# Performance work log

Measured on AMD Instinct MI355X. Metric: run time of the kernel, lower is better.

Reference implementation:

```python
import jax, jax.numpy as jnp
import numpy as np
from jax.scipy.special import logsumexp

B, K = 256, 6144            # batch, info block length (n = 3K, rate 1/3)
NUM_ITER = 6
MU = 3                      # memory of RSC code (constraint_length 4)
NS = 1 << MU                # 8 trellis states
G0 = (1, 0, 1, 1)           # feedback polynomial '1011'
G1 = (1, 1, 0, 1)           # output polynomial  '1101'
NEG = -1e30


def _build_trellis():
    nxt = np.zeros((NS, 2), np.int32)
    par = np.zeros((NS, 2), np.int32)
    for s in range(NS):
        r = [(s >> (MU - 1 - j)) & 1 for j in range(MU)]  # r[0] newest register bit
        for u in (0, 1):
            fb = (u + sum(G0[j + 1] * r[j] for j in range(MU))) % 2
            p = (G1[0] * fb + sum(G1[j + 1] * r[j] for j in range(MU))) % 2
            nxt[s, u] = (fb << (MU - 1)) | (s >> 1)
            par[s, u] = p
    prev_s = np.zeros((NS, 2), np.int32)
    prev_u = np.zeros((NS, 2), np.int32)
    cnt = np.zeros(NS, np.int32)
    for s in range(NS):
        for u in (0, 1):
            sn = nxt[s, u]
            prev_s[sn, cnt[sn]] = s
            prev_u[sn, cnt[sn]] = u
            cnt[sn] += 1
    return nxt, par, prev_s, prev_u

_NXT, _PAR, _PREV_S, _PREV_U = _build_trellis()


def bcjr(l_sys, l_par, l_a):
    """log-MAP BCJR on the rate-1/2 RSC trellis. LLR convention log p(0)/p(1).
    l_sys, l_par, l_a: [B, K] -> posterior LLR [B, K]."""
    nxt = jnp.asarray(_NXT)
    prev_s = jnp.asarray(_PREV_S)
    prev_u = jnp.asarray(_PREV_U)
    par_sign = jnp.asarray(1.0 - 2.0 * _PAR, l_sys.dtype)  # [NS,2]
    u_sign = jnp.asarray([1.0, -1.0], l_sys.dtype)         # (1-2u)
    b = l_sys.shape[0]
    lsu = (l_sys + l_a).T                                  # [K,B]
    lp = l_par.T
    # branch metrics gamma[t, b, s, u] = 0.5*((1-2u)(Lsys+La) + (1-2p)Lpar)
    gamma = 0.5 * (lsu[:, :, None, None] * u_sign + lp[:, :, None, None] * par_sign)
    alpha0 = jnp.full((b, NS), NEG, l_sys.dtype).at[:, 0].set(0.0)  # start in state 0

    def fwd(alpha, g):
        a = logsumexp(alpha[:, prev_s] + g[:, prev_s, prev_u], axis=-1)  # [B,NS]
        a = a - jnp.max(a, axis=-1, keepdims=True)
        return a, alpha

    _, alphas = jax.lax.scan(fwd, alpha0, gamma)           # alphas[t] = alpha_t  [K,B,NS]
    beta_end = jnp.zeros((b, NS), l_sys.dtype)             # unterminated: uniform

    def bwd(beta, g):
        bn = logsumexp(g + beta[:, nxt], axis=-1)          # [B,NS]
        bn = bn - jnp.max(bn, axis=-1, keepdims=True)
        return bn, beta

    _, betas1 = jax.lax.scan(bwd, beta_end, gamma, reverse=True)  # betas1[t] = beta_{t+1}
    m = alphas[..., None] + gamma + betas1[:, :, nxt]      # [K,B,NS,2]
    l_post = logsumexp(m[..., 0], axis=-1) - logsumexp(m[..., 1], axis=-1)  # [K,B]
    return l_post.T


def turbo_decode(inputs, perm):
    llr = -inputs                 # sionna logits log p1/p0 -> internal LLR log p0/p1
    ls1 = llr[:, 0::3]            # systematic
    lp1 = llr[:, 1::3]            # parity of encoder 1
    lp2 = llr[:, 2::3]            # parity of encoder 2
    ls2 = ls1[:, perm]            # interleaved systematic for decoder 2
    inv = jnp.argsort(perm)       # deinterleave index
    le2_de = jnp.zeros_like(ls1)
    for _ in range(NUM_ITER):
        la1 = le2_de
        lpost1 = bcjr(ls1, lp1, la1)
        le1 = lpost1 - la1 - ls1                  # extrinsic of decoder 1
        la2 = le1[:, perm]
        lpost2 = bcjr(ls2, lp2, la2)
        le2_de = (lpost2 - la2 - ls2)[:, inv]     # deinterleaved extrinsic of decoder 2
    return -lpost2[:, inv]        # soft output, back to logit convention (hard_out=False)


def setup_inputs() -> dict:
    key = jax.random.key(0)
    k1, k2 = jax.random.split(key)
    inputs = jax.random.normal(k1, (B, 3 * K), dtype=jnp.float32)
    perm = jax.random.permutation(k2, K)
    return {"inputs": inputs, "perm": perm}


def reference(inputs, perm):
    return turbo_decode(inputs, perm)
```

## Files before the change

### kernel.cpp

```cpp
#include <hip/hip_runtime.h>
#include <hip/hip_fp16.h>

constexpr int B_ = 256;
constexpr int K_ = 6144;
constexpr int NITER = 6;
constexpr int L_ = 6;
constexpr int W0_ = 6;
constexpr int C_ = K_ / L_;
constexpr int CPB = 4;
constexpr int GRID = C_ / CPB;
constexpr float LOG2E = 1.4426950408889634f;
constexpr float LN2   = 0.6931471805599453f;

static_assert(K_ % L_ == 0, "");
static_assert((L_ % 2) == 0 && (W0_ % 2) == 0, "");
static_assert(W0_ <= L_, "uniform-warmup trick requires W0 <= L");
static_assert(C_ % CPB == 0, "");

#if __has_builtin(__builtin_amdgcn_exp2f)
#define EXP2F(x) __builtin_amdgcn_exp2f(x)
#else
#define EXP2F(x) exp2f(x)
#endif
#if __has_builtin(__builtin_amdgcn_logf)
#define LOG2F(x) __builtin_amdgcn_logf(x)
#else
#define LOG2F(x) log2f(x)
#endif
#if __has_builtin(__builtin_amdgcn_rcpf)
#define RCPF(x) __builtin_amdgcn_rcpf(x)
#else
#define RCPF(x) (1.0f / (x))
#endif

__device__ __forceinline__ float b2f(unsigned short u) {
  return __uint_as_float((unsigned)u << 16);
}
__device__ __forceinline__ unsigned short f2b(float f) {
  unsigned u = __float_as_uint(f);
  u += 0x7FFFu + ((u >> 16) & 1u);
  return (unsigned short)(u >> 16);
}
__device__ __forceinline__ float h2f_bits(unsigned short us) {
  __half_raw r; r.x = us; return __half2float(__half(r));
}
__device__ __forceinline__ unsigned short f2h_bits(float f) {
  return __half_as_ushort(__float2half(f));
}

__device__ __forceinline__ unsigned int ld_dev_u32(const unsigned int* p) {
  return __hip_atomic_load(const_cast<unsigned int*>(p), __ATOMIC_RELAXED,
                           __HIP_MEMORY_SCOPE_AGENT);
}
__device__ __forceinline__ void st_dev_u32(unsigned int* p, unsigned int v) {
  __hip_atomic_store(p, v, __ATOMIC_RELAXED, __HIP_MEMORY_SCOPE_AGENT);
}
__device__ __forceinline__ float ld_dev_f32(const float* p) {
  return __hip_atomic_load(const_cast<float*>(p), __ATOMIC_RELAXED,
                           __HIP_MEMORY_SCOPE_AGENT);
}
__device__ __forceinline__ void st_dev_f32(float* p, float v) {
  __hip_atomic_store(p, v, __ATOMIC_RELAXED, __HIP_MEMORY_SCOPE_AGENT);
}
__device__ __forceinline__ unsigned long long ld_dev_u64(
    const unsigned long long* p) {
  return __hip_atomic_load(const_cast<unsigned long long*>(p),
                           __ATOMIC_RELAXED, __HIP_MEMORY_SCOPE_AGENT);
}
__device__ __forceinline__ void st_dev_u64(unsigned long long* p,
                                           unsigned long long v) {
  __hip_atomic_store(p, v, __ATOMIC_RELAXED, __HIP_MEMORY_SCOPE_AGENT);
}

__device__ __forceinline__ void gam_lin(float gxv, float gyv, float g[4]) {
  float es = EXP2F(-fabsf(gxv));
  float ep = EXP2F(-fabsf(gyv));
  float fu0 = gxv >= 0.0f ? 1.0f : es;
  float fu1 = gxv >= 0.0f ? es : 1.0f;
  float fp0 = gyv >= 0.0f ? 1.0f : ep;
  float fp1 = gyv >= 0.0f ? ep : 1.0f;
  g[0] = fu0 * fp0; g[1] = fu0 * fp1;
  g[2] = fu1 * fp0; g[3] = fu1 * fp1;
}

__device__ __forceinline__ void step_fwd_lin(float a[8], const float g[4]) {
  float an[8];
#pragma unroll
  for (int sn = 0; sn < 8; ++sn) {
    const int u0 = ((sn >> 2) ^ (sn & 1)) & 1;
    const int p0 = ((sn >> 2) ^ ((sn >> 1) & 1)) & 1;
    an[sn] = a[(sn & 3) * 2] * g[u0 * 2 + p0]
           + a[(sn & 3) * 2 + 1] * g[(u0 ^ 1) * 2 + (p0 ^ 1)];
  }
#pragma unroll
  for (int s = 0; s < 8; ++s) a[s] = an[s];
}

__device__ __forceinline__ void step_bwd_lin(float bt[8], const float g[4]) {
  float bn[8];
#pragma unroll
  for (int s = 0; s < 8; ++s) {
    const int s0 = s & 1, s1b = (s >> 1) & 1, s2b = (s >> 2) & 1;
    const int f0 = s1b ^ s0, q = s1b ^ s2b;
    bn[s] = g[q] * bt[(f0 << 2) | (s >> 1)]
          + g[2 + (q ^ 1)] * bt[((f0 ^ 1) << 2) | (s >> 1)];
  }
#pragma unroll
  for (int s = 0; s < 8; ++s) bt[s] = bn[s];
}

__device__ __forceinline__ void renorm_lin(float a[8]) {
  float m = fmaxf(fmaxf(fmaxf(a[0], a[1]), fmaxf(a[2], a[3])),
                  fmaxf(fmaxf(a[4], a[5]), fmaxf(a[6], a[7])));
  float r = RCPF(fmaxf(m, 1e-30f));
#pragma unroll
  for (int s = 0; s < 8; ++s) a[s] = fmaf(a[s], r, 1e-32f);
}

__device__ __forceinline__ unsigned long long pack8_log8(const float a[8]) {
  unsigned int us[8];
#pragma unroll
  for (int s = 0; s < 8; ++s) {
    float l = -16.0f * LOG2F(a[s]);
    l = fminf(l, 255.0f);
    us[s] = (unsigned int)(l + 0.5f);
  }
  unsigned int x = us[0] | (us[1] << 8) | (us[2] << 16) | (us[3] << 24);
  unsigned int y = us[4] | (us[5] << 8) | (us[6] << 16) | (us[7] << 24);
  return ((unsigned long long)y << 32) | x;
}

__device__ __forceinline__ void unpack8_log8(unsigned long long v, float a[8]) {
  unsigned int vx = (unsigned int)v, vy = (unsigned int)(v >> 32);
#pragma unroll
  for (int s = 0; s < 4; ++s)
    a[s] = EXP2F(-0.0625f * (float)((vx >> (8 * s)) & 0xFFu));
#pragma unroll
  for (int s = 0; s < 4; ++s)
    a[4 + s] = EXP2F(-0.0625f * (float)((vy >> (8 * s)) & 0xFFu));
}

constexpr int NSLOT = 2 * NITER;
constexpr int SLOT_U = 65 * 32;
constexpr int BARS_U = 28672;

__device__ __forceinline__ void tree_barrier(unsigned int* slotBase,
                                             unsigned int gsz) {
  __syncthreads();
  if (threadIdx.x == 0) {
    asm volatile("s_waitcnt vmcnt(0)" ::: "memory");
    const unsigned int g = blockIdx.x & 31u;
    unsigned int* cnt = slotBase + g * 32;
    unsigned int* rel = slotBase + (32 + g) * 32;
    unsigned int* root = slotBase + 64 * 32;
    unsigned int m = __hip_atomic_fetch_add(cnt, 1u, __ATOMIC_RELAXED,
                                            __HIP_MEMORY_SCOPE_AGENT);
    if (m == gsz - 1u) {
      unsigned int r = __hip_atomic_fetch_add(root, 1u, __ATOMIC_RELAXED,
                                              __HIP_MEMORY_SCOPE_AGENT);
      if (r == 31u) {
#pragma unroll
        for (int gg = 0; gg < 32; ++gg)
          st_dev_u32(slotBase + (32 + gg) * 32, 1u);
      }
    }
    while (!ld_dev_u32(rel))
      __builtin_amdgcn_s_sleep(2);
  }
  __syncthreads();
}

struct WSL {
  float* lpostT;
  __half* gx1; __half* gx2;
  unsigned short* gy1; unsigned short* gy2;
  __half* ls1; __half* ls2;
  int* inv;
  unsigned int* bars;
  unsigned long long *S1a, *S1b, *T1a, *T1b, *S2a, *S2b, *T2a, *T2b;
};

__host__ __device__ inline WSL ws_layout(char* ws) {
  const size_t KB = (size_t)K_ * B_;
  WSL w; char* p = ws;
  w.lpostT = (float*)p;            p += KB * 4;
  w.gx1    = (__half*)p;           p += KB * 2;
  w.gx2    = (__half*)p;           p += KB * 2;
  w.gy1    = (unsigned short*)p;   p += KB * 2;
  w.gy2    = (unsigned short*)p;   p += KB * 2;
  w.ls1    = (__half*)p;           p += KB * 2;
  w.ls2    = (__half*)p;           p += KB * 2;
  w.inv    = (int*)p;              p += (size_t)K_ * 4;
  w.bars   = (unsigned int*)p;     p += (size_t)BARS_U * 4;
  const size_t SB = (size_t)(C_ + 1) * B_;
  w.S1a = (unsigned long long*)p;  p += SB * 8;
  w.S1b = (unsigned long long*)p;  p += SB * 8;
  w.T1a = (unsigned long long*)p;  p += SB * 8;
  w.T1b = (unsigned long long*)p;  p += SB * 8;
  w.S2a = (unsigned long long*)p;  p += SB * 8;
  w.S2b = (unsigned long long*)p;  p += SB * 8;
  w.T2a = (unsigned long long*)p;  p += SB * 8;
  w.T2b = (unsigned long long*)p;  p += SB * 8;
  return w;
}

template <bool DEV>
__device__ __forceinline__ void half_body(
    const int c,
    const __half* __restrict__ gx,
    const unsigned short* __restrict__ gy,
    const __half* __restrict__ lsloc,
    const int* __restrict__ map,
    __half* __restrict__ gxother,
    float* __restrict__ lpost_out,
    const unsigned long long* __restrict__ Sread,
    unsigned long long* __restrict__ Swrite,
    const unsigned long long* __restrict__ Tread,
    unsigned long long* __restrict__ Twrite,
    const unsigned long long* lds_sr, unsigned long long* lds_sw,
    const unsigned long long* lds_tr, unsigned long long* lds_tw,
    int b, int wmode, int mode, int wrS, bool gxc) {
  const int kv = c * L_;
  const int kend = kv + L_;
  const unsigned int* gxp = (const unsigned int*)gx;
  const int bh = b >> 1;
  const unsigned int hsel = (b & 1) * 16;
  const bool gdev = DEV && !gxc;

  float gvx[L_];
  unsigned short rgy[L_];
  __half hls[L_];
#pragma unroll
  for (int i = 0; i < L_; ++i) {
    size_t o2 = (size_t)(kv + i) * (B_ / 2) + bh;
    unsigned int u = gdev ? ld_dev_u32(gxp + o2) : gxp[o2];
    gvx[i] = h2f_bits((unsigned short)(u >> hsel));
    rgy[i] = gy[(size_t)(kv + i) * B_ + b];
  }
  if (mode == 0) {
#pragma unroll
    for (int i = 0; i < L_; ++i)
      hls[i] = lsloc[(size_t)(kv + i) * B_ + b];
  }
  int jmap[L_];
#pragma unroll
  for (int i = 0; i < L_; ++i) jmap[i] = map[kv + i];
  unsigned long long sraw = 0, traw = 0;
  float wfx[W0_], wbx[W0_];
  unsigned short wfy[W0_], wby[W0_];
  if (wmode == 2) {
    if (c > 0) {
      if (lds_sr) sraw = *lds_sr;
      else {
        const size_t o = (size_t)c * B_ + b;
        sraw = DEV ? ld_dev_u64(Sread + o) : Sread[o];
      }
    }
    if (c < C_ - 1) {
      if (lds_tr) traw = *lds_tr;
      else {
        const size_t o = (size_t)(c + 1) * B_ + b;
        traw = DEV ? ld_dev_u64(Tread + o) : Tread[o];
      }
    }
  } else {
    if (c > 0) {
#pragma unroll
      for (int q = 0; q < W0_; ++q) {
        size_t o2 = (size_t)(kv - W0_ + q) * (B_ / 2) + bh;
        unsigned int u = gdev ? ld_dev_u32(gxp + o2) : gxp[o2];
        wfx[q] = h2f_bits((unsigned short)(u >> hsel));
        wfy[q] = gy[(size_t)(kv - W0_ + q) * B_ + b];
      }
    }
    if (c < C_ - 1) {
#pragma unroll
      for (int q = 0; q < W0_; ++q) {
        size_t o2 = (size_t)(kend + W0_ - 1 - q) * (B_ / 2) + bh;
        unsigned int u = gdev ? ld_dev_u32(gxp + o2) : gxp[o2];
        wbx[q] = h2f_bits((unsigned short)(u >> hsel));
        wby[q] = gy[(size_t)(kend + W0_ - 1 - q) * B_ + b];
      }
    }
  }

  float gc[L_][4];
#pragma unroll
  for (int i = 0; i < L_; ++i) gam_lin(gvx[i], b2f(rgy[i]), gc[i]);

  float a[8];
  if (c == 0) {
    a[0] = 1.0f;
#pragma unroll
    for (int s = 1; s < 8; ++s) a[s] = 0.0f;
  } else if (wmode == 0) {
    if (c == 1) {
      a[0] = 1.0f;
#pragma unroll
      for (int s = 1; s < 8; ++s) a[s] = 0.0f;
    } else {
#pragma unroll
      for (int s = 0; s < 8; ++s) a[s] = 1.0f;
    }
#pragma unroll
    for (int q = 0; q < W0_; ++q) {
      float g[4];
      gam_lin(wfx[q], b2f(wfy[q]), g);
      step_fwd_lin(a, g);
      if (q & 1) renorm_lin(a);
    }
  } else {
    unpack8_log8(sraw, a);
  }
  float a2d[L_][8];
#pragma unroll
  for (int i = 0; i < L_; ++i) {
#pragma unroll
    for (int s = 0; s < 8; ++s) a2d[i][s] = a[s];
    step_fwd_lin(a, gc[i]);
    if (i & 1) renorm_lin(a);
  }
  if (wrS) {
    unsigned long long v = pack8_log8(a);
    if (lds_sw) *lds_sw = v;
    else {
      unsigned long long* p = Swrite + (size_t)(c + 1) * B_ + b;
      if (DEV) st_dev_u64(p, v); else *p = v;
    }
  }

  float bt[8];
  if (c == C_ - 1) {
#pragma unroll
    for (int s = 0; s < 8; ++s) bt[s] = 1.0f;
  } else if (wmode == 0) {
#pragma unroll
    for (int s = 0; s < 8; ++s) bt[s] = 1.0f;
#pragma unroll
    for (int q = 0; q < W0_; ++q) {
      float g[4];
      gam_lin(wbx[q], b2f(wby[q]), g);
      step_bwd_lin(bt, g);
      if (q & 1) renorm_lin(bt);
    }
  } else {
    unpack8_log8(traw, bt);
  }
#pragma unroll
  for (int ii = 0; ii < L_; ++ii) {
    const int i = L_ - 1 - ii;
    const float* g = gc[i];
    float s00 = 0.0f, s01 = 0.0f, s10 = 0.0f, s11 = 0.0f;
    float bn[8];
#pragma unroll
    for (int s = 0; s < 8; ++s) {
      const int s0 = s & 1, s1b = (s >> 1) & 1, s2b = (s >> 2) & 1;
      const int f0 = s1b ^ s0, q = s1b ^ s2b;
      float b0 = bt[(f0 << 2) | (s >> 1)];
      float b1 = bt[((f0 ^ 1) << 2) | (s >> 1)];
      float m0 = a2d[i][s] * b0;
      float m1 = a2d[i][s] * b1;
      if (q == 0) { s00 += m0; s10 += m1; } else { s01 += m0; s11 += m1; }
      bn[s] = g[q] * b0 + g[2 + (q ^ 1)] * b1;
    }
    float t0 = g[0] * s00 + g[1] * s01;
    float t1 = g[3] * s10 + g[2] * s11;
    float lpost = LOG2F(fmaxf(t0, 1e-37f)) - LOG2F(fmaxf(t1, 1e-37f));
    if (mode == 0) {
      float le = lpost - gvx[i];
      unsigned short us = f2h_bits(__half2float(hls[i]) + le);
      unsigned int po = (unsigned int)__shfl_xor((int)us, 1);
      unsigned int u32v = (b & 1) ? (po | ((unsigned int)us << 16))
                                  : ((unsigned int)us | (po << 16));
      unsigned int uhi = (unsigned int)__shfl_xor((int)u32v, 2);
      if ((b & 3) == 0) {
        unsigned long long v64 =
            (unsigned long long)u32v | ((unsigned long long)uhi << 32);
        unsigned long long* p =
            (unsigned long long*)gxother + ((size_t)jmap[i] * (B_ / 4) + (b >> 2));
        if (DEV) st_dev_u64(p, v64); else *p = v64;
      }
    } else {
      float v = -LN2 * lpost;
      float* p = lpost_out + ((size_t)jmap[i] * B_ + b);
      if (DEV) st_dev_f32(p, v); else *p = v;
    }
#pragma unroll
    for (int s = 0; s < 8; ++s) bt[s] = bn[s];
    if (ii & 1) renorm_lin(bt);
  }
  if (wrS) {
    unsigned long long v = pack8_log8(bt);
    if (lds_tw) *lds_tw = v;
    else {
      unsigned long long* p = Twrite + (size_t)c * B_ + b;
      if (DEV) st_dev_u64(p, v); else *p = v;
    }
  }
}

__global__ __launch_bounds__(1024, 4) void k_fused(const int* __restrict__ perm,
                                                   float* __restrict__ out,
                                                   char* __restrict__ ws) {
  WSL w = ws_layout(ws);
  __shared__ unsigned long long ldsST[2][2][2][3][256];
  const int tid = threadIdx.x;
  const int q = tid >> 8;
  const int b = tid & 255;
  const int c = blockIdx.x * CPB + q;
  const unsigned int gsz = gridDim.x >> 5;

#pragma unroll
  for (int r = 0; r < L_; ++r) {
    const int j = c * L_ + r;
    w.ls2[(size_t)j * B_ + b] = w.ls1[(size_t)perm[j] * B_ + b];
  }

  int slot = 0;
  for (int it = 0; it < NITER; ++it) {
    const int pr = it & 1, pw = pr ^ 1;
    const int wm = (it == 0) ? 0 : 2;
    const int wrS = (it != NITER - 1) ? 1 : 0;
    unsigned long long* S1r = pr ? w.S1b : w.S1a;
    unsigned long long* S1w = pr ? w.S1a : w.S1b;
    unsigned long long* T1r = pr ? w.T1b : w.T1a;
    unsigned long long* T1w = pr ? w.T1a : w.T1b;
    unsigned long long* S2r = pr ? w.S2b : w.S2a;
    unsigned long long* S2w = pr ? w.S2a : w.S2b;
    unsigned long long* T2r = pr ? w.T2b : w.T2a;
    unsigned long long* T2w = pr ? w.T2a : w.T2b;
    half_body<true>(c, w.gx1, w.gy1, w.ls1, w.inv, w.gx2, w.lpostT,
                    S1r, S1w, T1r, T1w,
                    (q > 0) ? &ldsST[0][0][pr][q - 1][b] : nullptr,
                    (q < 3) ? &ldsST[0][0][pw][q][b] : nullptr,
                    (q < 3) ? &ldsST[1][0][pr][q][b] : nullptr,
                    (q > 0) ? &ldsST[1][0][pw][q - 1][b] : nullptr,
                    b, wm, 0, wrS, it == 0);
    tree_barrier(w.bars + slot * SLOT_U, gsz); ++slot;
    half_body<true>(c, w.gx2, w.gy2, w.ls2, perm, w.gx1, w.lpostT,
                    S2r, S2w, T2r, T2w,
                    (q > 0) ? &ldsST[0][1][pr][q - 1][b] : nullptr,
                    (q < 3) ? &ldsST[0][1][pw][q][b] : nullptr,
                    (q < 3) ? &ldsST[1][1][pr][q][b] : nullptr,
                    (q > 0) ? &ldsST[1][1][pw][q - 1][b] : nullptr,
                    b, wm, (it == NITER - 1) ? 1 : 0, wrS, false);
    tree_barrier(w.bars + slot * SLOT_U, gsz); ++slot;
  }

  float* tt = reinterpret_cast<float*>(&ldsST[0][0][0][0][0]);
  for (int t = blockIdx.x; t < (K_ / 64) * (B_ / 64); t += gridDim.x) {
    const int i0 = (t >> 2) * 64;
    const int b0 = (t & 3) * 64;
    __syncthreads();
    const int tb = tid & 63, iq = tid >> 6;
    for (int ii = iq; ii < 64; ii += 16)
      tt[ii * 65 + tb] =
          ld_dev_f32(w.lpostT + (size_t)(i0 + ii) * B_ + (b0 + tb));
    __syncthreads();
    for (int bb = iq; bb < 64; bb += 16)
      out[(size_t)(b0 + bb) * K_ + (i0 + tb)] = tt[tb * 65 + bb];
  }
}

__global__ __launch_bounds__(256, 4) void k_half(
    const __half* __restrict__ gx, const unsigned short* __restrict__ gy,
    const __half* __restrict__ lsloc, const int* __restrict__ map,
    __half* __restrict__ gxother, float* __restrict__ lpost_out,
    const unsigned long long* __restrict__ Sread,
    unsigned long long* __restrict__ Swrite,
    const unsigned long long* __restrict__ Tread,
    unsigned long long* __restrict__ Twrite,
    int wmode, int mode, int wrS) {
  half_body<false>(blockIdx.x, gx, gy, lsloc, map, gxother, lpost_out,
                   Sread, Swrite, Tread, Twrite,
                   nullptr, nullptr, nullptr, nullptr,
                   threadIdx.x, wmode, mode, wrS, true);
}

__global__ __launch_bounds__(256) void k_prep2(const __half* __restrict__ ls1,
                                               const int* __restrict__ perm,
                                               __half* __restrict__ ls2) {
  const int b = threadIdx.x;
#pragma unroll
  for (int r = 0; r < 8; ++r) {
    const int j = blockIdx.x * 8 + r;
    ls2[(size_t)j * B_ + b] = ls1[(size_t)perm[j] * B_ + b];
  }
}

__global__ __launch_bounds__(256) void k_out(const float* __restrict__ lpostT,
                                             float* __restrict__ out) {
  __shared__ float t[64][65];
  const int tid = threadIdx.x;
  const int i0 = blockIdx.x * 64, b0 = blockIdx.y * 64;
  const int tb = tid & 63, iq = tid >> 6;
  for (int ii = iq; ii < 64; ii += 4) {
    t[ii][tb] = lpostT[(size_t)(i0 + ii) * B_ + (b0 + tb)];
  }
  __syncthreads();
  const int ik = tid & 63, bq = tid >> 6;
  for (int bb = bq; bb < 64; bb += 4) {
    out[(size_t)(b0 + bb) * K_ + (i0 + ik)] = t[ik][bb];
  }
}

__global__ __launch_bounds__(256) void k_prep1(const float* __restrict__ inp,
                                               const int* __restrict__ perm,
                                               __half* __restrict__ gx1,
                                               __half* __restrict__ ls1,
                                               unsigned short* __restrict__ gy1,
                                               unsigned short* __restrict__ gy2,
                                               int* __restrict__ inv,
                                               unsigned int* __restrict__ bars) {
  __shared__ float t[3][64][65];
  const int tid = threadIdx.x;
  const int k0 = blockIdx.x * 64, b0 = blockIdx.y * 64;
  const int tk = tid & 63, tq = tid >> 6;
  for (int bb = tq; bb < 64; bb += 4) {
    size_t base = (size_t)(b0 + bb) * (3 * K_) + 3 * (size_t)(k0 + tk);
    t[0][bb][tk] = inp[base + 0];
    t[1][bb][tk] = inp[base + 1];
    t[2][bb][tk] = inp[base + 2];
  }
  __syncthreads();
  const int tb = tid & 63, kq = tid >> 6;
  for (int kk = kq; kk < 64; kk += 4) {
    size_t o = (size_t)(k0 + kk) * B_ + (b0 + tb);
    float sv = -LOG2E * t[0][tb][kk];
    float p1 = -LOG2E * t[1][tb][kk];
    float p2 = -LOG2E * t[2][tb][kk];
    ls1[o] = __float2half(sv);
    gy1[o] = f2b(p1);
    gy2[o] = f2b(p2);
    if (!(tb & 1)) {
      float sv1 = -LOG2E * t[0][tb + 1][kk];
      unsigned int u = (unsigned int)f2h_bits(sv) |
                       ((unsigned int)f2h_bits(sv1) << 16);
      ((unsigned int*)gx1)[o >> 1] = u;
    }
  }
  if (blockIdx.y == 0 && tid < 64) {
    const int j = k0 + tid;
    inv[perm[j]] = j;
  }
  if (blockIdx.y == 1 && blockIdx.x < BARS_U / 1024) {
#pragma unroll
    for (int r = 0; r < 4; ++r)
      bars[(size_t)blockIdx.x * 1024 + r * 256 + tid] = 0;
  }
}

static void launch_fallback(const int* perm, float* out, char* wsb,
                            hipStream_t stream) {
  WSL w = ws_layout(wsb);
  k_prep2<<<K_ / 8, 256, 0, stream>>>(w.ls1, perm, w.ls2);
  for (int it = 0; it < NITER; ++it) {
    const int pr = it & 1;
    const int wm = (it == 0) ? 0 : 2;
    const int wrS = (it != NITER - 1) ? 1 : 0;
    unsigned long long* S1r = pr ? w.S1b : w.S1a;
    unsigned long long* S1w = pr ? w.S1a : w.S1b;
    unsigned long long* T1r = pr ? w.T1b : w.T1a;
    unsigned long long* T1w = pr ? w.T1a : w.T1b;
    unsigned long long* S2r = pr ? w.S2b : w.S2a;
    unsigned long long* S2w = pr ? w.S2a : w.S2b;
    unsigned long long* T2r = pr ? w.T2b : w.T2a;
    unsigned long long* T2w = pr ? w.T2a : w.T2b;
    k_half<<<C_, 256, 0, stream>>>(w.gx1, w.gy1, w.ls1, w.inv, w.gx2,
                                   w.lpostT, S1r, S1w, T1r, T1w, wm, 0, wrS);
    k_half<<<C_, 256, 0, stream>>>(w.gx2, w.gy2, w.ls2, perm, w.gx1,
                                   w.lpostT, S2r, S2w, T2r, T2w, wm,
                                   (it == NITER - 1) ? 1 : 0, wrS);
  }
  k_out<<<dim3(K_ / 64, B_ / 64), 256, 0, stream>>>(w.lpostT, out);
}

extern "C" void kernel_launch(void* const* d_in, const int* in_sizes, int n_in,
                              void* d_out, int out_size, void* d_ws, size_t ws_size,
                              hipStream_t stream) {
  (void)in_sizes; (void)n_in; (void)out_size; (void)ws_size;
  const float* inp = (const float*)d_in[0];
  const int* perm = (const int*)d_in[1];
  float* out = (float*)d_out;
  char* wsb = (char*)d_ws;
  WSL w = ws_layout(wsb);

  k_prep1<<<dim3(K_ / 64, B_ / 64), 256, 0, stream>>>(
      inp, perm, w.gx1, w.ls1, w.gy1, w.gy2, w.inv, w.bars);

  static int g_mode = 0;

  if (g_mode == 0) {
    int nb = 0;
    if (hipOccupancyMaxActiveBlocksPerMultiprocessor(&nb, k_fused, 1024, 0)
            != hipSuccess)
      nb = 0;
    int ncu = 0;
    hipDeviceProp_t prop;
    int dev = 0;
    (void)hipGetDevice(&dev);
    if (hipGetDeviceProperties(&prop, dev) == hipSuccess)
      ncu = prop.multiProcessorCount;
    g_mode = ((long long)nb * ncu >= GRID && (GRID % 32) == 0) ? 1 : 2;
  }

  if (g_mode == 1) {
    k_fused<<<GRID, 1024, 0, stream>>>(perm, out, wsb);
  } else {
    launch_fallback(perm, out, wsb, stream);
  }
}
```

Measured before the change: 212.7 us.

## Fuse input prep into persistent kernel and read permuted systematic LLRs directly

Moves the input transpose/quantise prep stage into the persistent fused kernel, behind an extra grid barrier, and zeroes the barrier slots with a memset instead of in the prep kernel. It drops the precomputed interleaved systematic array and instead gathers rows of ls1 through the permutation inside decoder 2. Intra-block state handoff through LDS now stores fp16 pairs instead of 8-bit log-quantised values, with an added block sync. The barrier spin sleep is also shortened. This removes a kernel launch and a full ls2 write/read, at the cost of uncoalesced gathered loads in decoder 2 and an extra barrier plus a __syncthreads per half-iteration.

```diff
diff --git a/kernel.cpp b/kernel.cpp
--- a/kernel.cpp
+++ b/kernel.cpp
@@ -9,6 +9,7 @@
 constexpr int C_ = K_ / L_;
 constexpr int CPB = 4;
 constexpr int GRID = C_ / CPB;
+constexpr int NTILE = (K_ / 64) * (B_ / 64);
 constexpr float LOG2E = 1.4426950408889634f;
 constexpr float LN2   = 0.6931471805599453f;
 
@@ -140,7 +141,28 @@
     a[4 + s] = EXP2F(-0.0625f * (float)((vy >> (8 * s)) & 0xFFu));
 }
 
-constexpr int NSLOT = 2 * NITER;
+__device__ __forceinline__ void pack8_h(const float a[8],
+                                        unsigned long long o[2]) {
+  unsigned int u[4];
+#pragma unroll
+  for (int k = 0; k < 4; ++k)
+    u[k] = (unsigned int)f2h_bits(a[2 * k]) |
+           ((unsigned int)f2h_bits(a[2 * k + 1]) << 16);
+  o[0] = (unsigned long long)u[0] | ((unsigned long long)u[1] << 32);
+  o[1] = (unsigned long long)u[2] | ((unsigned long long)u[3] << 32);
+}
+__device__ __forceinline__ void unpack8_h(unsigned long long v0,
+                                          unsigned long long v1, float a[8]) {
+  unsigned int u[4] = {(unsigned int)v0, (unsigned int)(v0 >> 32),
+                       (unsigned int)v1, (unsigned int)(v1 >> 32)};
+#pragma unroll
+  for (int k = 0; k < 4; ++k) {
+    a[2 * k] = h2f_bits((unsigned short)u[k]);
+    a[2 * k + 1] = h2f_bits((unsigned short)(u[k] >> 16));
+  }
+}
+
+constexpr int NSLOT = 2 * NITER + 1;
 constexpr int SLOT_U = 65 * 32;
 constexpr int BARS_U = 28672;
 
@@ -165,7 +187,7 @@
       }
     }
     while (!ld_dev_u32(rel))
-      __builtin_amdgcn_s_sleep(2);
+      __builtin_amdgcn_s_sleep(1);
   }
   __syncthreads();
 }
@@ -174,7 +196,7 @@
   float* lpostT;
   __half* gx1; __half* gx2;
   unsigned short* gy1; unsigned short* gy2;
-  __half* ls1; __half* ls2;
+  __half* ls1;
   int* inv;
   unsigned int* bars;
   unsigned long long *S1a, *S1b, *T1a, *T1b, *S2a, *S2b, *T2a, *T2b;
@@ -189,7 +211,6 @@
   w.gy1    = (unsigned short*)p;   p += KB * 2;
   w.gy2    = (unsigned short*)p;   p += KB * 2;
   w.ls1    = (__half*)p;           p += KB * 2;
-  w.ls2    = (__half*)p;           p += KB * 2;
   w.inv    = (int*)p;              p += (size_t)K_ * 4;
   w.bars   = (unsigned int*)p;     p += (size_t)BARS_U * 4;
   const size_t SB = (size_t)(C_ + 1) * B_;
@@ -219,7 +240,7 @@
     unsigned long long* __restrict__ Twrite,
     const unsigned long long* lds_sr, unsigned long long* lds_sw,
     const unsigned long long* lds_tr, unsigned long long* lds_tw,
-    int b, int wmode, int mode, int wrS, bool gxc) {
+    int b, int wmode, int mode, int wrS, bool gxc, bool lsmapped) {
   const int kv = c * L_;
   const int kend = kv + L_;
   const unsigned int* gxp = (const unsigned int*)gx;
@@ -227,6 +248,9 @@
   const unsigned int hsel = (b & 1) * 16;
   const bool gdev = DEV && !gxc;
 
+  int jmap[L_];
+#pragma unroll
+  for (int i = 0; i < L_; ++i) jmap[i] = map[kv + i];
   float gvx[L_];
   unsigned short rgy[L_];
   __half hls[L_];
@@ -239,28 +263,28 @@
   }
   if (mode == 0) {
 #pragma unroll
-    for (int i = 0; i < L_; ++i)
-      hls[i] = lsloc[(size_t)(kv + i) * B_ + b];
-  }
-  int jmap[L_];
-#pragma unroll
-  for (int i = 0; i < L_; ++i) jmap[i] = map[kv + i];
-  unsigned long long sraw = 0, traw = 0;
+    for (int i = 0; i < L_; ++i) {
+      const size_t lrow = lsmapped ? (size_t)jmap[i] : (size_t)(kv + i);
+      hls[i] = lsloc[lrow * B_ + b];
+    }
+  }
+  unsigned long long sA = 0, sB = 0, tA = 0, tB = 0;
+  bool s_lds = false, t_lds = false;
   float wfx[W0_], wbx[W0_];
   unsigned short wfy[W0_], wby[W0_];
   if (wmode == 2) {
     if (c > 0) {
-      if (lds_sr) sraw = *lds_sr;
+      if (DEV && lds_sr) { sA = lds_sr[0]; sB = lds_sr[1]; s_lds = true; }
       else {
         const size_t o = (size_t)c * B_ + b;
-        sraw = DEV ? ld_dev_u64(Sread + o) : Sread[o];
+        sA = DEV ? ld_dev_u64(Sread + o) : Sread[o];
       }
     }
     if (c < C_ - 1) {
-      if (lds_tr) traw = *lds_tr;
+      if (DEV && lds_tr) { tA = lds_tr[0]; tB = lds_tr[1]; t_lds = true; }
       else {
         const size_t o = (size_t)(c + 1) * B_ + b;
-        traw = DEV ? ld_dev_u64(Tread + o) : Tread[o];
+        tA = DEV ? ld_dev_u64(Tread + o) : Tread[o];
       }
     }
   } else {
@@ -283,6 +307,7 @@
       }
     }
   }
+  if (DEV) __syncthreads();
 
   float gc[L_][4];
 #pragma unroll
@@ -310,7 +335,7 @@
       if (q & 1) renorm_lin(a);
     }
   } else {
-    unpack8_log8(sraw, a);
+    if (s_lds) unpack8_h(sA, sB, a); else unpack8_log8(sA, a);
   }
   float a2d[L_][8];
 #pragma unroll
@@ -321,9 +346,10 @@
     if (i & 1) renorm_lin(a);
   }
   if (wrS) {
-    unsigned long long v = pack8_log8(a);
-    if (lds_sw) *lds_sw = v;
-    else {
+    if (DEV && lds_sw) {
+      pack8_h(a, lds_sw);
+    } else {
+      unsigned long long v = pack8_log8(a);
       unsigned long long* p = Swrite + (size_t)(c + 1) * B_ + b;
       if (DEV) st_dev_u64(p, v); else *p = v;
     }
@@ -344,7 +370,7 @@
       if (q & 1) renorm_lin(bt);
     }
   } else {
-    unpack8_log8(traw, bt);
+    if (t_lds) unpack8_h(tA, tB, bt); else unpack8_log8(tA, bt);
   }
 #pragma unroll
   for (int ii = 0; ii < L_; ++ii) {
@@ -390,35 +416,72 @@
     if (ii & 1) renorm_lin(bt);
   }
   if (wrS) {
-    unsigned long long v = pack8_log8(bt);
-    if (lds_tw) *lds_tw = v;
-    else {
+    if (DEV && lds_tw) {
+      pack8_h(bt, lds_tw);
+    } else {
+      unsigned long long v = pack8_log8(bt);
       unsigned long long* p = Twrite + (size_t)c * B_ + b;
       if (DEV) st_dev_u64(p, v); else *p = v;
     }
   }
 }
 
-__global__ __launch_bounds__(1024, 4) void k_fused(const int* __restrict__ perm,
-                                                   float* __restrict__ out,
-                                                   char* __restrict__ ws) {
+__global__ __launch_bounds__(1024) void k_fused(const float* __restrict__ inp,
+                                                const int* __restrict__ perm,
+                                                float* __restrict__ out,
+                                                char* __restrict__ ws) {
   WSL w = ws_layout(ws);
-  __shared__ unsigned long long ldsST[2][2][2][3][256];
+  __shared__ __align__(16) char ldsraw[3 * 64 * 65 * 4];
   const int tid = threadIdx.x;
   const int q = tid >> 8;
   const int b = tid & 255;
   const int c = blockIdx.x * CPB + q;
   const unsigned int gsz = gridDim.x >> 5;
 
-#pragma unroll
-  for (int r = 0; r < L_; ++r) {
-    const int j = c * L_ + r;
-    w.ls2[(size_t)j * B_ + b] = w.ls1[(size_t)perm[j] * B_ + b];
-  }
-
-  int slot = 0;
+  {
+    float (*tp)[64][65] = (float(*)[64][65])ldsraw;
+    for (int t = blockIdx.x; t < NTILE; t += gridDim.x) {
+      const int k0 = (t % 96) * 64, b0 = (t / 96) * 64;
+      __syncthreads();
+      const int tk = tid & 63;
+      for (int bb = tid >> 6; bb < 64; bb += 16) {
+        size_t base = (size_t)(b0 + bb) * (3 * K_) + 3 * (size_t)(k0 + tk);
+        tp[0][bb][tk] = inp[base + 0];
+        tp[1][bb][tk] = inp[base + 1];
+        tp[2][bb][tk] = inp[base + 2];
+      }
+      __syncthreads();
+      const int tb = tid & 63;
+      if (!(tb & 1)) {
+        for (int kk = tid >> 6; kk < 64; kk += 16) {
+          size_t o = (size_t)(k0 + kk) * B_ + (b0 + tb);
+          float sv0 = -LOG2E * tp[0][tb][kk];
+          float sv1 = -LOG2E * tp[0][tb + 1][kk];
+          unsigned int uls = (unsigned int)f2h_bits(sv0) |
+                             ((unsigned int)f2h_bits(sv1) << 16);
+          unsigned int ug1 = (unsigned int)f2b(-LOG2E * tp[1][tb][kk]) |
+                             ((unsigned int)f2b(-LOG2E * tp[1][tb + 1][kk]) << 16);
+          unsigned int ug2 = (unsigned int)f2b(-LOG2E * tp[2][tb][kk]) |
+                             ((unsigned int)f2b(-LOG2E * tp[2][tb + 1][kk]) << 16);
+          st_dev_u32((unsigned int*)w.ls1 + (o >> 1), uls);
+          st_dev_u32((unsigned int*)w.gx1 + (o >> 1), uls);
+          st_dev_u32((unsigned int*)w.gy1 + (o >> 1), ug1);
+          st_dev_u32((unsigned int*)w.gy2 + (o >> 1), ug2);
+        }
+      }
+      if (t < 96 && tid < 64)
+        st_dev_u32((unsigned int*)w.inv + perm[k0 + tid],
+                   (unsigned int)(k0 + tid));
+    }
+  }
+  tree_barrier(w.bars + 0 * SLOT_U, gsz);
+
+  unsigned long long* stbase = (unsigned long long*)ldsraw;
+#define STSLOT(st, d, bb) (stbase + ((((st) * 2 + (d)) * 3 + (bb)) * 256 + b) * 2)
+
+  int slot = 1;
   for (int it = 0; it < NITER; ++it) {
-    const int pr = it & 1, pw = pr ^ 1;
+    const int pr = it & 1;
     const int wm = (it == 0) ? 0 : 2;
     const int wrS = (it != NITER - 1) ? 1 : 0;
     unsigned long long* S1r = pr ? w.S1b : w.S1a;
@@ -431,24 +494,25 @@
     unsigned long long* T2w = pr ? w.T2a : w.T2b;
     half_body<true>(c, w.gx1, w.gy1, w.ls1, w.inv, w.gx2, w.lpostT,
                     S1r, S1w, T1r, T1w,
-                    (q > 0) ? &ldsST[0][0][pr][q - 1][b] : nullptr,
-                    (q < 3) ? &ldsST[0][0][pw][q][b] : nullptr,
-                    (q < 3) ? &ldsST[1][0][pr][q][b] : nullptr,
-                    (q > 0) ? &ldsST[1][0][pw][q - 1][b] : nullptr,
-                    b, wm, 0, wrS, it == 0);
+                    (q > 0) ? STSLOT(0, 0, q - 1) : nullptr,
+                    (q < 3) ? STSLOT(0, 0, q) : nullptr,
+                    (q < 3) ? STSLOT(1, 0, q) : nullptr,
+                    (q > 0) ? STSLOT(1, 0, q - 1) : nullptr,
+                    b, wm, 0, wrS, it == 0, false);
     tree_barrier(w.bars + slot * SLOT_U, gsz); ++slot;
-    half_body<true>(c, w.gx2, w.gy2, w.ls2, perm, w.gx1, w.lpostT,
+    half_body<true>(c, w.gx2, w.gy2, w.ls1, perm, w.gx1, w.lpostT,
                     S2r, S2w, T2r, T2w,
-                    (q > 0) ? &ldsST[0][1][pr][q - 1][b] : nullptr,
-                    (q < 3) ? &ldsST[0][1][pw][q][b] : nullptr,
-                    (q < 3) ? &ldsST[1][1][pr][q][b] : nullptr,
-                    (q > 0) ? &ldsST[1][1][pw][q - 1][b] : nullptr,
-                    b, wm, (it == NITER - 1) ? 1 : 0, wrS, false);
+                    (q > 0) ? STSLOT(0, 1, q - 1) : nullptr,
+                    (q < 3) ? STSLOT(0, 1, q) : nullptr,
+                    (q < 3) ? STSLOT(1, 1, q) : nullptr,
+                    (q > 0) ? STSLOT(1, 1, q - 1) : nullptr,
+                    b, wm, (it == NITER - 1) ? 1 : 0, wrS, false, true);
     tree_barrier(w.bars + slot * SLOT_U, gsz); ++slot;
   }
-
-  float* tt = reinterpret_cast<float*>(&ldsST[0][0][0][0][0]);
-  for (int t = blockIdx.x; t < (K_ / 64) * (B_ / 64); t += gridDim.x) {
+#undef STSLOT
+
+  float* tt = (float*)ldsraw;
+  for (int t = blockIdx.x; t < NTILE; t += gridDim.x) {
     const int i0 = (t >> 2) * 64;
     const int b0 = (t & 3) * 64;
     __syncthreads();
@@ -470,22 +534,11 @@
     unsigned long long* __restrict__ Swrite,
     const unsigned long long* __restrict__ Tread,
     unsigned long long* __restrict__ Twrite,
-    int wmode, int mode, int wrS) {
+    int wmode, int mode, int wrS, int lsmapped) {
   half_body<false>(blockIdx.x, gx, gy, lsloc, map, gxother, lpost_out,
                    Sread, Swrite, Tread, Twrite,
                    nullptr, nullptr, nullptr, nullptr,
-                   threadIdx.x, wmode, mode, wrS, true);
-}
-
-__global__ __launch_bounds__(256) void k_prep2(const __half* __restrict__ ls1,
-                                               const int* __restrict__ perm,
-                                               __half* __restrict__ ls2) {
-  const int b = threadIdx.x;
-#pragma unroll
-  for (int r = 0; r < 8; ++r) {
-    const int j = blockIdx.x * 8 + r;
-    ls2[(size_t)j * B_ + b] = ls1[(size_t)perm[j] * B_ + b];
-  }
+                   threadIdx.x, wmode, mode, wrS, true, lsmapped != 0);
 }
 
 __global__ __launch_bounds__(256) void k_out(const float* __restrict__ lpostT,
@@ -510,8 +563,7 @@
                                                __half* __restrict__ ls1,
                                                unsigned short* __restrict__ gy1,
                                                unsigned short* __restrict__ gy2,
-                                               int* __restrict__ inv,
-                                               unsigned int* __restrict__ bars) {
+                                               int* __restrict__ inv) {
   __shared__ float t[3][64][65];
   const int tid = threadIdx.x;
   const int k0 = blockIdx.x * 64, b0 = blockIdx.y * 64;
@@ -527,11 +579,9 @@
   for (int kk = kq; kk < 64; kk += 4) {
     size_t o = (size_t)(k0 + kk) * B_ + (b0 + tb);
     float sv = -LOG2E * t[0][tb][kk];
-    float p1 = -LOG2E * t[1][tb][kk];
-    float p2 = -LOG2E * t[2][tb][kk];
     ls1[o] = __float2half(sv);
-    gy1[o] = f2b(p1);
-    gy2[o] = f2b(p2);
+    gy1[o] = f2b(-LOG2E * t[1][tb][kk]);
+    gy2[o] = f2b(-LOG2E * t[2][tb][kk]);
     if (!(tb & 1)) {
       float sv1 = -LOG2E * t[0][tb + 1][kk];
       unsigned int u = (unsigned int)f2h_bits(sv) |
@@ -543,17 +593,13 @@
     const int j = k0 + tid;
     inv[perm[j]] = j;
   }
-  if (blockIdx.y == 1 && blockIdx.x < BARS_U / 1024) {
-#pragma unroll
-    for (int r = 0; r < 4; ++r)
-      bars[(size_t)blockIdx.x * 1024 + r * 256 + tid] = 0;
-  }
-}
-
-static void launch_fallback(const int* perm, float* out, char* wsb,
-                            hipStream_t stream) {
+}
+
+static void launch_fallback(const float* inp, const int* perm, float* out,
+                            char* wsb, hipStream_t stream) {
   WSL w = ws_layout(wsb);
-  k_prep2<<<K_ / 8, 256, 0, stream>>>(w.ls1, perm, w.ls2);
+  k_prep1<<<dim3(K_ / 64, B_ / 64), 256, 0, stream>>>(
+      inp, perm, w.gx1, w.ls1, w.gy1, w.gy2, w.inv);
   for (int it = 0; it < NITER; ++it) {
     const int pr = it & 1;
     const int wm = (it == 0) ? 0 : 2;
@@ -567,10 +613,11 @@
     unsigned long long* T2r = pr ? w.T2b : w.T2a;
     unsigned long long* T2w = pr ? w.T2a : w.T2b;
     k_half<<<C_, 256, 0, stream>>>(w.gx1, w.gy1, w.ls1, w.inv, w.gx2,
-                                   w.lpostT, S1r, S1w, T1r, T1w, wm, 0, wrS);
-    k_half<<<C_, 256, 0, stream>>>(w.gx2, w.gy2, w.ls2, perm, w.gx1,
+                                   w.lpostT, S1r, S1w, T1r, T1w, wm, 0, wrS,
+                                   0);
+    k_half<<<C_, 256, 0, stream>>>(w.gx2, w.gy2, w.ls1, perm, w.gx1,
                                    w.lpostT, S2r, S2w, T2r, T2w, wm,
-                                   (it == NITER - 1) ? 1 : 0, wrS);
+                                   (it == NITER - 1) ? 1 : 0, wrS, 1);
   }
   k_out<<<dim3(K_ / 64, B_ / 64), 256, 0, stream>>>(w.lpostT, out);
 }
@@ -584,9 +631,6 @@
   float* out = (float*)d_out;
   char* wsb = (char*)d_ws;
   WSL w = ws_layout(wsb);
-
-  k_prep1<<<dim3(K_ / 64, B_ / 64), 256, 0, stream>>>(
-      inp, perm, w.gx1, w.ls1, w.gy1, w.gy2, w.inv, w.bars);
 
   static int g_mode = 0;
 
@@ -605,8 +649,9 @@
   }
 
   if (g_mode == 1) {
-    k_fused<<<GRID, 1024, 0, stream>>>(perm, out, wsb);
+    (void)hipMemsetAsync(w.bars, 0, (size_t)BARS_U * 4, stream);
+    k_fused<<<GRID, 1024, 0, stream>>>(inp, perm, out, wsb);
   } else {
-    launch_fallback(perm, out, wsb, stream);
-  }
-}
+    launch_fallback(inp, perm, out, wsb, stream);
+  }
+}
```

Result: no change. 210.5 us (-1.0%).
